# Performance work log

Hardware: AMD Instinct MI355X
Metric: run time of the kernel (lower is better)

The kernel has to match this reference:

```python
import jax, jax.numpy as jnp
import numpy as np

# Model/config constants (match init_kwargs)
B, S, D, H = 2, 2048, 512, 8
HD = D // H            # head dim = 64
WIN, DIL, G = 16, 2, 64  # window size, dilation rate, num global tokens
L = S - G              # 1984 local tokens (global indices are 0..G-1)


def setup_inputs() -> dict:
    key = jax.random.key(0)
    ks = jax.random.split(key, 16)
    sc = 0.02
    n = jax.random.normal
    return {
        "query": n(ks[0], (B, S, D), jnp.float32),
        "key": n(ks[1], (B, S, D), jnp.float32),
        "value": n(ks[2], (B, S, D), jnp.float32),
        # local multi-head attention params (linear_query/key/value/out_proj)
        "wq": n(ks[3], (D, D), jnp.float32) * sc, "bq": jnp.zeros((D,), jnp.float32),
        "wk": n(ks[4], (D, D), jnp.float32) * sc, "bk": jnp.zeros((D,), jnp.float32),
        "wv": n(ks[5], (D, D), jnp.float32) * sc, "bv": jnp.zeros((D,), jnp.float32),
        "wo": n(ks[6], (D, D), jnp.float32) * sc, "bo": jnp.zeros((D,), jnp.float32),
        # global nn.MultiheadAttention params (packed in_proj + out_proj)
        "g_in_w": n(ks[7], (3 * D, D), jnp.float32) * sc,
        "g_in_b": jnp.zeros((3 * D,), jnp.float32),
        "g_out_w": n(ks[8], (D, D), jnp.float32) * sc,
        "g_out_b": jnp.zeros((D,), jnp.float32),
    }


def _window_indices():
    # centered dilated window per local position, clipped to valid range
    pos = jnp.arange(L)
    offs = DIL * (jnp.arange(WIN) - WIN // 2)
    return jnp.clip(pos[:, None] + offs[None, :], 0, L - 1)


def reference(query, key, value, wq, bq, wk, bk, wv, bv, wo, bo,
              g_in_w, g_in_b, g_out_w, g_out_b):
    scale = 1.0 / np.sqrt(HD).astype(np.float32)

    # ---- local (dilated sliding window) path over tokens G..S-1 ----
    q_loc = query[:, G:, :]                      # (B, L, D)
    widx = _window_indices()
    k_win = key[:, G:, :][:, widx, :]
    v_win = value[:, G:, :][:, widx, :]

    q = (q_loc @ wq.T + bq).reshape(B, L, H, HD)          # (B,L,H,HD)
    k = (k_win @ wk.T + bk).reshape(B, L, WIN, H, HD)     # (B,L,W,H,HD)
    v = (v_win @ wv.T + bv).reshape(B, L, WIN, H, HD)

    scores = jnp.einsum('blhd,blwhd->blhw', q, k) * scale
    p = jax.nn.softmax(scores, axis=-1)
    o = jnp.einsum('blhw,blwhd->blhd', p, v).reshape(B, L, D)
    local_out = o @ wo.T + bo                              # (B,L,D)

    # ---- global token path: standard MHA over the G global tokens ----
    wq_g, wk_g, wv_g = g_in_w[:D], g_in_w[D:2 * D], g_in_w[2 * D:]
    bq_g, bk_g, bv_g = g_in_b[:D], g_in_b[D:2 * D], g_in_b[2 * D:]
    qg = (query[:, :G] @ wq_g.T + bq_g).reshape(B, G, H, HD)
    kg = (key[:, :G] @ wk_g.T + bk_g).reshape(B, G, H, HD)
    vg = (value[:, :G] @ wv_g.T + bv_g).reshape(B, G, H, HD)
    sg = jnp.einsum('bqhd,bkhd->bhqk', qg, kg) * scale     # (B,H,G,G)
    pg = jax.nn.softmax(sg, axis=-1)
    og = jnp.einsum('bhqk,bkhd->bqhd', pg, vg).reshape(B, G, D)
    global_out = og @ g_out_w.T + g_out_b                  # (B,G,D)

    # ---- fuse: scatter local + global back into full sequence ----
    out = jnp.zeros((B, S, D), query.dtype)
    out = out.at[:, G:, :].set(local_out)
    out = out.at[:, :G, :].set(global_out)
    return out
```

## Files before the change

### kernel.cpp

```cpp
#include <hip/hip_runtime.h>
#include <stdint.h>

#define B_ 2
#define S_ 2048
#define D_ 512
#define H_ 8
#define WIN_ 16
#define DIL_ 2
#define G_ 64
#define L_ (S_ - G_)

typedef short bf16x8 __attribute__((ext_vector_type(8)));
typedef float f32x4 __attribute__((ext_vector_type(4)));
typedef unsigned short u16;

#define LDSW 40

__device__ __forceinline__ float bf2f(u16 h) {
  return __uint_as_float(((uint32_t)h) << 16);
}
__device__ __forceinline__ u16 f2bf(float f) {
  uint32_t u = __float_as_uint(f);
  uint32_t r = (u + 0x7fffu + ((u >> 16) & 1u)) >> 16;
  return (u16)r;
}
__device__ __forceinline__ uint32_t pack2(float lo, float hi) {
  return (uint32_t)f2bf(lo) | ((uint32_t)f2bf(hi) << 16);
}

struct Job {
  const void* X; const float* W; const float* bias; void* Y;
  int rpb;
  int xoff;
  long xbs;
  int yoff;
  long ybs;
  int out_f32;
};
struct GemmLaunch { int start[6]; Job job[6]; };

template <int X_BF16>
__global__ __launch_bounds__(256) void gemm_kernel(GemmLaunch a) {
  int bid = (int)blockIdx.x;
  bid = (bid & 7) * ((int)gridDim.x >> 3) + (bid >> 3);

  int j = 0;
#pragma unroll
  for (int i = 1; i < 6; ++i) j = (bid >= a.start[i]) ? i : j;
  const Job jb = a.job[j];
  bid -= a.start[j];
  const int tm = bid >> 3, tn = bid & 7;
  const int row0 = tm * 128, n0 = tn * 64;

  __shared__ __align__(16) u16 As[2][128 * LDSW];
  __shared__ __align__(16) u16 Bs[2][64 * LDSW];

  const int tid = threadIdx.x, lane = tid & 63, w = tid >> 6;
  const int wm = w >> 1, wn = w & 1;

  const int rs = tid >> 2;
  const int kq = (tid & 3) * 8;

  const int r0 = row0 + rs,      b0 = r0 >= jb.rpb;
  const int r1 = row0 + 64 + rs, b1 = r1 >= jb.rpb;
  const size_t xi0 = (size_t)(b0 ? jb.xbs : 0) +
                     (size_t)(jb.xoff + r0 - (b0 ? jb.rpb : 0)) * 512 + kq;
  const size_t xi1 = (size_t)(b1 ? jb.xbs : 0) +
                     (size_t)(jb.xoff + r1 - (b1 ? jb.rpb : 0)) * 512 + kq;
  const float* wb0 = jb.W + (size_t)(n0 + rs) * 512 + kq;

  f32x4 acc[4][2];
#pragma unroll
  for (int i = 0; i < 4; ++i)
#pragma unroll
    for (int k = 0; k < 2; ++k) acc[i][k] = (f32x4){0.f, 0.f, 0.f, 0.f};

  f32x4 Aa0, Aa1, Aa2, Aa3, Aw0, Aw1;
  f32x4 Ba0, Ba1, Ba2, Ba3, Bw0, Bw1;
  int4  Ax0, Ax1, Bx0, Bx1;

  auto issueA = [&](int kof) {
    if constexpr (X_BF16) {
      const u16* xb = (const u16*)jb.X;
      Ax0 = *(const int4*)&xb[xi0 + kof];
      Ax1 = *(const int4*)&xb[xi1 + kof];
    } else {
      const float* xf = (const float*)jb.X;
      Aa0 = *(const f32x4*)(xf + xi0 + kof);
      Aa1 = *(const f32x4*)(xf + xi0 + kof + 4);
      Aa2 = *(const f32x4*)(xf + xi1 + kof);
      Aa3 = *(const f32x4*)(xf + xi1 + kof + 4);
    }
    Aw0 = *(const f32x4*)(wb0 + kof);
    Aw1 = *(const f32x4*)(wb0 + kof + 4);
  };
  auto issueB = [&](int kof) {
    if constexpr (X_BF16) {
      const u16* xb = (const u16*)jb.X;
      Bx0 = *(const int4*)&xb[xi0 + kof];
      Bx1 = *(const int4*)&xb[xi1 + kof];
    } else {
      const float* xf = (const float*)jb.X;
      Ba0 = *(const f32x4*)(xf + xi0 + kof);
      Ba1 = *(const f32x4*)(xf + xi0 + kof + 4);
      Ba2 = *(const f32x4*)(xf + xi1 + kof);
      Ba3 = *(const f32x4*)(xf + xi1 + kof + 4);
    }
    Bw0 = *(const f32x4*)(wb0 + kof);
    Bw1 = *(const f32x4*)(wb0 + kof + 4);
  };
  auto writeA = [&](int buf) {
    if constexpr (X_BF16) {
      *(int4*)&As[buf][rs * LDSW + kq]        = Ax0;
      *(int4*)&As[buf][(64 + rs) * LDSW + kq] = Ax1;
    } else {
      int4 p;
      p.x = (int)pack2(Aa0[0], Aa0[1]); p.y = (int)pack2(Aa0[2], Aa0[3]);
      p.z = (int)pack2(Aa1[0], Aa1[1]); p.w = (int)pack2(Aa1[2], Aa1[3]);
      *(int4*)&As[buf][rs * LDSW + kq] = p;
      p.x = (int)pack2(Aa2[0], Aa2[1]); p.y = (int)pack2(Aa2[2], Aa2[3]);
      p.z = (int)pack2(Aa3[0], Aa3[1]); p.w = (int)pack2(Aa3[2], Aa3[3]);
      *(int4*)&As[buf][(64 + rs) * LDSW + kq] = p;
    }
    int4 pw;
    pw.x = (int)pack2(Aw0[0], Aw0[1]); pw.y = (int)pack2(Aw0[2], Aw0[3]);
    pw.z = (int)pack2(Aw1[0], Aw1[1]); pw.w = (int)pack2(Aw1[2], Aw1[3]);
    *(int4*)&Bs[buf][rs * LDSW + kq] = pw;
  };
  auto writeB = [&](int buf) {
    if constexpr (X_BF16) {
      *(int4*)&As[buf][rs * LDSW + kq]        = Bx0;
      *(int4*)&As[buf][(64 + rs) * LDSW + kq] = Bx1;
    } else {
      int4 p;
      p.x = (int)pack2(Ba0[0], Ba0[1]); p.y = (int)pack2(Ba0[2], Ba0[3]);
      p.z = (int)pack2(Ba1[0], Ba1[1]); p.w = (int)pack2(Ba1[2], Ba1[3]);
      *(int4*)&As[buf][rs * LDSW + kq] = p;
      p.x = (int)pack2(Ba2[0], Ba2[1]); p.y = (int)pack2(Ba2[2], Ba2[3]);
      p.z = (int)pack2(Ba3[0], Ba3[1]); p.w = (int)pack2(Ba3[2], Ba3[3]);
      *(int4*)&As[buf][(64 + rs) * LDSW + kq] = p;
    }
    int4 pw;
    pw.x = (int)pack2(Bw0[0], Bw0[1]); pw.y = (int)pack2(Bw0[2], Bw0[3]);
    pw.z = (int)pack2(Bw1[0], Bw1[1]); pw.w = (int)pack2(Bw1[2], Bw1[3]);
    *(int4*)&Bs[buf][rs * LDSW + kq] = pw;
  };
  auto compute = [&](int buf) {
    bf16x8 af[4], bfv[2];
#pragma unroll
    for (int fm = 0; fm < 4; ++fm)
      af[fm] = *(const bf16x8*)&As[buf][(wm * 64 + fm * 16 + (lane & 15)) * LDSW + 8 * (lane >> 4)];
#pragma unroll
    for (int fn = 0; fn < 2; ++fn)
      bfv[fn] = *(const bf16x8*)&Bs[buf][(wn * 32 + fn * 16 + (lane & 15)) * LDSW + 8 * (lane >> 4)];
#pragma unroll
    for (int fm = 0; fm < 4; ++fm)
#pragma unroll
      for (int fn = 0; fn < 2; ++fn)
        acc[fm][fn] = __builtin_amdgcn_mfma_f32_16x16x32_bf16(af[fm], bfv[fn], acc[fm][fn], 0, 0, 0);
  };

  issueA(0);
  issueB(32);
  writeA(0);
  __syncthreads();
  for (int t = 0; t < 14; t += 2) {
    issueA((t + 2) * 32);
    compute(0);
    writeB(1);
    __syncthreads();
    issueB((t + 3) * 32);
    compute(1);
    writeA(0);
    __syncthreads();
  }
  compute(0);
  writeB(1);
  __syncthreads();
  compute(1);

#pragma unroll
  for (int fm = 0; fm < 4; ++fm) {
#pragma unroll
    for (int fn = 0; fn < 2; ++fn) {
#pragma unroll
      for (int r = 0; r < 4; ++r) {
        const int row = row0 + wm * 64 + fm * 16 + (lane >> 4) * 4 + r;
        const int col = n0 + wn * 32 + fn * 16 + (lane & 15);
        const int b = row >= jb.rpb;
        const int rr = row - (b ? jb.rpb : 0);
        const size_t yi = (size_t)(b ? jb.ybs : 0) + (size_t)(jb.yoff + rr) * 512 + col;
        const float v = acc[fm][fn][r] + jb.bias[col];
        if (jb.out_f32) ((float*)jb.Y)[yi] = v;
        else            ((u16*)jb.Y)[yi]   = f2bf(v);
      }
    }
  }
}

__global__ __launch_bounds__(256) void attn_kernel(const u16* qp, const u16* kp,
                                                   const u16* vp, u16* ob,
                                                   const u16* qgp, const u16* kgp,
                                                   const u16* vgp, u16* ogp) {
  const int lane = threadIdx.x & 63;
  int bid = (int)blockIdx.x;
  const int nbl = (B_ * L_) / 4;
  if (bid < nbl) bid = (bid & 7) * (nbl >> 3) + (bid >> 3);
  const int wid = bid * 4 + (threadIdx.x >> 6);

  if (wid < B_ * L_) {
    const int l = wid % L_;
    const int brow = wid - l;
    float q[8];
    {
      bf16x8 qv = *(const bf16x8*)&qp[(size_t)wid * 512 + lane * 8];
#pragma unroll
      for (int e = 0; e < 8; ++e) q[e] = bf2f((u16)qv[e]);
    }
    float s[WIN_];
#pragma unroll
    for (int w2 = 0; w2 < WIN_; ++w2) {
      int ki = l + DIL_ * w2 - WIN_;
      ki = ki < 0 ? 0 : (ki > L_ - 1 ? L_ - 1 : ki);
      bf16x8 kv = *(const bf16x8*)&kp[(size_t)(brow + ki) * 512 + lane * 8];
      float p = 0.f;
#pragma unroll
      for (int e = 0; e < 8; ++e) p = fmaf(q[e], bf2f((u16)kv[e]), p);
      p += __shfl_xor(p, 1); p += __shfl_xor(p, 2); p += __shfl_xor(p, 4);
      s[w2] = p * 0.125f;
    }
    float m = s[0];
#pragma unroll
    for (int w2 = 1; w2 < WIN_; ++w2) m = fmaxf(m, s[w2]);
    float sum = 0.f;
#pragma unroll
    for (int w2 = 0; w2 < WIN_; ++w2) { s[w2] = __expf(s[w2] - m); sum += s[w2]; }
    const float inv = 1.0f / sum;
    float acc[8] = {0.f};
#pragma unroll
    for (int w2 = 0; w2 < WIN_; ++w2) {
      int ki = l + DIL_ * w2 - WIN_;
      ki = ki < 0 ? 0 : (ki > L_ - 1 ? L_ - 1 : ki);
      bf16x8 vv = *(const bf16x8*)&vp[(size_t)(brow + ki) * 512 + lane * 8];
#pragma unroll
      for (int e = 0; e < 8; ++e) acc[e] = fmaf(s[w2], bf2f((u16)vv[e]), acc[e]);
    }
    bf16x8 o8;
#pragma unroll
    for (int e = 0; e < 8; ++e) o8[e] = (short)f2bf(acc[e] * inv);
    *(bf16x8*)&ob[(size_t)wid * 512 + lane * 8] = o8;
  } else {
    const int g = wid - B_ * L_;
    const int base = (g >> 6) * 64;
    const int qi = g & 63;
    float q[8];
    {
      bf16x8 qv = *(const bf16x8*)&qgp[(size_t)(base + qi) * 512 + lane * 8];
#pragma unroll
      for (int e = 0; e < 8; ++e) q[e] = bf2f((u16)qv[e]);
    }
    float m = -1e30f, sum = 0.f, acc[8] = {0.f};
    for (int j2 = 0; j2 < 64; ++j2) {
      bf16x8 kv = *(const bf16x8*)&kgp[(size_t)(base + j2) * 512 + lane * 8];
      float p = 0.f;
#pragma unroll
      for (int e = 0; e < 8; ++e) p = fmaf(q[e], bf2f((u16)kv[e]), p);
      p += __shfl_xor(p, 1); p += __shfl_xor(p, 2); p += __shfl_xor(p, 4);
      p *= 0.125f;
      const float mn = fmaxf(m, p);
      const float c  = __expf(m - mn);
      const float pe = __expf(p - mn);
      sum = sum * c + pe;
      m = mn;
      bf16x8 vv = *(const bf16x8*)&vgp[(size_t)(base + j2) * 512 + lane * 8];
#pragma unroll
      for (int e = 0; e < 8; ++e) acc[e] = acc[e] * c + pe * bf2f((u16)vv[e]);
    }
    const float inv = 1.0f / sum;
    bf16x8 o8;
#pragma unroll
    for (int e = 0; e < 8; ++e) o8[e] = (short)f2bf(acc[e] * inv);
    *(bf16x8*)&ogp[(size_t)(base + qi) * 512 + lane * 8] = o8;
  }
}

extern "C" void kernel_launch(void* const* d_in, const int* in_sizes, int n_in,
                              void* d_out, int out_size, void* d_ws, size_t ws_size,
                              hipStream_t stream) {
  const float* query   = (const float*)d_in[0];
  const float* key     = (const float*)d_in[1];
  const float* value   = (const float*)d_in[2];
  const float* wq      = (const float*)d_in[3];
  const float* bq      = (const float*)d_in[4];
  const float* wk      = (const float*)d_in[5];
  const float* bk      = (const float*)d_in[6];
  const float* wv      = (const float*)d_in[7];
  const float* bv      = (const float*)d_in[8];
  const float* wo      = (const float*)d_in[9];
  const float* bo      = (const float*)d_in[10];
  const float* g_in_w  = (const float*)d_in[11];
  const float* g_in_b  = (const float*)d_in[12];
  const float* g_out_w = (const float*)d_in[13];
  const float* g_out_b = (const float*)d_in[14];
  float* out = (float*)d_out;

  u16* w16 = (u16*)d_ws;
  const size_t PSZ = (size_t)B_ * L_ * D_;
  const size_t GSZ = (size_t)B_ * G_ * D_;

  u16* qp  = w16;        u16* kp  = qp + PSZ;   u16* vp  = kp + PSZ;
  u16* ob  = vp + PSZ;
  u16* qgp = ob + PSZ;   u16* kgp = qgp + GSZ;  u16* vgp = kgp + GSZ;
  u16* ogp = vgp + GSZ;

  const long XBS = (long)S_ * D_;
  const long PBS = (long)L_ * D_;
  const long GBS = (long)G_ * D_;

  GemmLaunch gi;
  gi.start[0] = 0; gi.start[1] = 248; gi.start[2] = 496;
  gi.start[3] = 744; gi.start[4] = 752; gi.start[5] = 760;
  gi.job[0] = {query, wq, bq, qp, L_, G_, XBS, 0, PBS, 0};
  gi.job[1] = {key,   wk, bk, kp, L_, G_, XBS, 0, PBS, 0};
  gi.job[2] = {value, wv, bv, vp, L_, G_, XBS, 0, PBS, 0};
  gi.job[3] = {query, g_in_w,             g_in_b,          qgp, G_, 0, XBS, 0, GBS, 0};
  gi.job[4] = {key,   g_in_w + 512 * D_,  g_in_b + D_,     kgp, G_, 0, XBS, 0, GBS, 0};
  gi.job[5] = {value, g_in_w + 1024 * D_, g_in_b + 2 * D_, vgp, G_, 0, XBS, 0, GBS, 0};
  hipLaunchKernelGGL(gemm_kernel<0>, dim3(768), dim3(256), 0, stream, gi);

  hipLaunchKernelGGL(attn_kernel, dim3((B_ * L_ + 128) / 4), dim3(256), 0, stream,
                     qp, kp, vp, ob, qgp, kgp, vgp, ogp);

  GemmLaunch go;
  go.start[0] = 0; go.start[1] = 248;
  go.start[2] = go.start[3] = go.start[4] = go.start[5] = 0x7fffffff;
  go.job[0] = {ob,  wo,      bo,      out, L_, 0, PBS, G_, XBS, 1};
  go.job[1] = {ogp, g_out_w, g_out_b, out, G_, 0, GBS, 0,  XBS, 1};
  go.job[2] = go.job[1]; go.job[3] = go.job[1]; go.job[4] = go.job[1]; go.job[5] = go.job[1];
  hipLaunchKernelGGL(gemm_kernel<1>, dim3(256), dim3(256), 0, stream, go);
}
```

Before: 162.2 us.

## Widen input-projection GEMM tile to 128x128 with 512-thread blocks

Adds a WIDE template variant of the GEMM where each 512-thread block computes a 128x128 output tile, with eight waves arranged 2x4, instead of 128x64 with 256 threads. Each thread now loads one A row and one W row per stage. The QKV input projections use it with half as many blocks, which raises reuse of A per block and halves redundant fp32 A loads and bf16 conversions. The compute section and epilogue are not shown, so it is unclear whether they handle the 4-wide wn mapping correctly. Fewer, larger blocks may also lower occupancy.

After: 162.9 us. About the same (+0.4%).

```diff
diff --git a/kernel.cpp b/kernel.cpp
--- a/kernel.cpp
+++ b/kernel.cpp
@@ -39,8 +39,8 @@
 };
 struct GemmLaunch { int start[6]; Job job[6]; };
 
-template <int X_BF16>
-__global__ __launch_bounds__(256) void gemm_kernel(GemmLaunch a) {
+template <int X_BF16, int WIDE>
+__global__ __launch_bounds__(WIDE ? 512 : 256) void gemm_kernel(GemmLaunch a) {
   int bid = (int)blockIdx.x;
   bid = (bid & 7) * ((int)gridDim.x >> 3) + (bid >> 3);
 
@@ -49,22 +49,24 @@
   for (int i = 1; i < 6; ++i) j = (bid >= a.start[i]) ? i : j;
   const Job jb = a.job[j];
   bid -= a.start[j];
-  const int tm = bid >> 3, tn = bid & 7;
-  const int row0 = tm * 128, n0 = tn * 64;
+  const int tm = WIDE ? (bid >> 2) : (bid >> 3);
+  const int tn = WIDE ? (bid & 3) : (bid & 7);
+  const int row0 = tm * 128, n0 = tn * (WIDE ? 128 : 64);
 
   __shared__ __align__(16) u16 As[2][128 * LDSW];
-  __shared__ __align__(16) u16 Bs[2][64 * LDSW];
+  __shared__ __align__(16) u16 Bs[2][(WIDE ? 128 : 64) * LDSW];
 
   const int tid = threadIdx.x, lane = tid & 63, w = tid >> 6;
-  const int wm = w >> 1, wn = w & 1;
+  const int wm = WIDE ? (w >> 2) : (w >> 1);
+  const int wn = WIDE ? (w & 3) : (w & 1);
 
   const int rs = tid >> 2;
   const int kq = (tid & 3) * 8;
 
   const int r0 = row0 + rs,      b0 = r0 >= jb.rpb;
-  const int r1 = row0 + 64 + rs, b1 = r1 >= jb.rpb;
   const size_t xi0 = (size_t)(b0 ? jb.xbs : 0) +
                      (size_t)(jb.xoff + r0 - (b0 ? jb.rpb : 0)) * 512 + kq;
+  const int r1 = row0 + 64 + rs, b1 = r1 >= jb.rpb;
   const size_t xi1 = (size_t)(b1 ? jb.xbs : 0) +
                      (size_t)(jb.xoff + r1 - (b1 ? jb.rpb : 0)) * 512 + kq;
   const float* wb0 = jb.W + (size_t)(n0 + rs) * 512 + kq;
@@ -83,13 +85,15 @@
     if constexpr (X_BF16) {
       const u16* xb = (const u16*)jb.X;
       Ax0 = *(const int4*)&xb[xi0 + kof];
-      Ax1 = *(const int4*)&xb[xi1 + kof];
+      if constexpr (!WIDE) Ax1 = *(const int4*)&xb[xi1 + kof];
     } else {
       const float* xf = (const float*)jb.X;
       Aa0 = *(const f32x4*)(xf + xi0 + kof);
       Aa1 = *(const f32x4*)(xf + xi0 + kof + 4);
-      Aa2 = *(const f32x4*)(xf + xi1 + kof);
-      Aa3 = *(const f32x4*)(xf + xi1 + kof + 4);
+      if constexpr (!WIDE) {
+        Aa2 = *(const f32x4*)(xf + xi1 + kof);
+        Aa3 = *(const f32x4*)(xf + xi1 + kof + 4);
+      }
     }
     Aw0 = *(const f32x4*)(wb0 + kof);
     Aw1 = *(const f32x4*)(wb0 + kof + 4);
@@ -98,29 +102,33 @@
     if constexpr (X_BF16) {
       const u16* xb = (const u16*)jb.X;
       Bx0 = *(const int4*)&xb[xi0 + kof];
-      Bx1 = *(const int4*)&xb[xi1 + kof];
+      if constexpr (!WIDE) Bx1 = *(const int4*)&xb[xi1 + kof];
     } else {
       const float* xf = (const float*)jb.X;
       Ba0 = *(const f32x4*)(xf + xi0 + kof);
       Ba1 = *(const f32x4*)(xf + xi0 + kof + 4);
-      Ba2 = *(const f32x4*)(xf + xi1 + kof);
-      Ba3 = *(const f32x4*)(xf + xi1 + kof + 4);
+      if constexpr (!WIDE) {
+        Ba2 = *(const f32x4*)(xf + xi1 + kof);
+        Ba3 = *(const f32x4*)(xf + xi1 + kof + 4);
+      }
     }
     Bw0 = *(const f32x4*)(wb0 + kof);
     Bw1 = *(const f32x4*)(wb0 + kof + 4);
   };
   auto writeA = [&](int buf) {
     if constexpr (X_BF16) {
-      *(int4*)&As[buf][rs * LDSW + kq]        = Ax0;
-      *(int4*)&As[buf][(64 + rs) * LDSW + kq] = Ax1;
+      *(int4*)&As[buf][rs * LDSW + kq] = Ax0;
+      if constexpr (!WIDE) *(int4*)&As[buf][(64 + rs) * LDSW + kq] = Ax1;
     } else {
       int4 p;
       p.x = (int)pack2(Aa0[0], Aa0[1]); p.y = (int)pack2(Aa0[2], Aa0[3]);
       p.z = (int)pack2(Aa1[0], Aa1[1]); p.w = (int)pack2(Aa1[2], Aa1[3]);
       *(int4*)&As[buf][rs * LDSW + kq] = p;
-      p.x = (int)pack2(Aa2[0], Aa2[1]); p.y = (int)pack2(Aa2[2], Aa2[3]);
-      p.z = (int)pack2(Aa3[0], Aa3[1]); p.w = (int)pack2(Aa3[2], Aa3[3]);
-      *(int4*)&As[buf][(64 + rs) * LDSW + kq] = p;
+      if constexpr (!WIDE) {
+        p.x = (int)pack2(Aa2[0], Aa2[1]); p.y = (int)pack2(Aa2[2], Aa2[3]);
+        p.z = (int)pack2(Aa3[0], Aa3[1]); p.w = (int)pack2(Aa3[2], Aa3[3]);
+        *(int4*)&As[buf][(64 + rs) * LDSW + kq] = p;
+      }
     }
     int4 pw;
     pw.x = (int)pack2(Aw0[0], Aw0[1]); pw.y = (int)pack2(Aw0[2], Aw0[3]);
@@ -129,16 +137,18 @@
   };
   auto writeB = [&](int buf) {
     if constexpr (X_BF16) {
-      *(int4*)&As[buf][rs * LDSW + kq]        = Bx0;
-      *(int4*)&As[buf][(64 + rs) * LDSW + kq] = Bx1;
+      *(int4*)&As[buf][rs * LDSW + kq] = Bx0;
+      if constexpr (!WIDE) *(int4*)&As[buf][(64 + rs) * LDSW + kq] = Bx1;
     } else {
       int4 p;
       p.x = (int)pack2(Ba0[0], Ba0[1]); p.y = (int)pack2(Ba0[2], Ba0[3]);
       p.z = (int)pack2(Ba1[0], Ba1[1]); p.w = (int)pack2(Ba1[2], Ba1[3]);
       *(int4*)&As[buf][rs * LDSW + kq] = p;
-      p.x = (int)pack2(Ba2[0], Ba2[1]); p.y = (int)pack2(Ba2[2], Ba2[3]);
-      p.z = (int)pack2(Ba3[0], Ba3[1]); p.w = (int)pack2(Ba3[2], Ba3[3]);
-      *(int4*)&As[buf][(64 + rs) * LDSW + kq] = p;
+      if constexpr (!WIDE) {
+        p.x = (int)pack2(Ba2[0], Ba2[1]); p.y = (int)pack2(Ba2[2], Ba2[3]);
+        p.z = (int)pack2(Ba3[0], Ba3[1]); p.w = (int)pack2(Ba3[2], Ba3[3]);
+        *(int4*)&As[buf][(64 + rs) * LDSW + kq] = p;
+      }
     }
     int4 pw;
     pw.x = (int)pack2(Bw0[0], Bw0[1]); pw.y = (int)pack2(Bw0[2], Bw0[3]);
@@ -318,15 +328,15 @@
   const long GBS = (long)G_ * D_;
 
   GemmLaunch gi;
-  gi.start[0] = 0; gi.start[1] = 248; gi.start[2] = 496;
-  gi.start[3] = 744; gi.start[4] = 752; gi.start[5] = 760;
+  gi.start[0] = 0; gi.start[1] = 124; gi.start[2] = 248;
+  gi.start[3] = 372; gi.start[4] = 376; gi.start[5] = 380;
   gi.job[0] = {query, wq, bq, qp, L_, G_, XBS, 0, PBS, 0};
   gi.job[1] = {key,   wk, bk, kp, L_, G_, XBS, 0, PBS, 0};
   gi.job[2] = {value, wv, bv, vp, L_, G_, XBS, 0, PBS, 0};
   gi.job[3] = {query, g_in_w,             g_in_b,          qgp, G_, 0, XBS, 0, GBS, 0};
   gi.job[4] = {key,   g_in_w + 512 * D_,  g_in_b + D_,     kgp, G_, 0, XBS, 0, GBS, 0};
   gi.job[5] = {value, g_in_w + 1024 * D_, g_in_b + 2 * D_, vgp, G_, 0, XBS, 0, GBS, 0};
-  hipLaunchKernelGGL(gemm_kernel<0>, dim3(768), dim3(256), 0, stream, gi);
+  hipLaunchKernelGGL((gemm_kernel<0, 1>), dim3(384), dim3(512), 0, stream, gi);
 
   hipLaunchKernelGGL(attn_kernel, dim3((B_ * L_ + 128) / 4), dim3(256), 0, stream,
                      qp, kp, vp, ob, qgp, kgp, vgp, ogp);
@@ -337,5 +347,5 @@
   go.job[0] = {ob,  wo,      bo,      out, L_, 0, PBS, G_, XBS, 1};
   go.job[1] = {ogp, g_out_w, g_out_b, out, G_, 0, GBS, 0,  XBS, 1};
   go.job[2] = go.job[1]; go.job[3] = go.job[1]; go.job[4] = go.job[1]; go.job[5] = go.job[1];
-  hipLaunchKernelGGL(gemm_kernel<1>, dim3(256), dim3(256), 0, stream, go);
-}
+  hipLaunchKernelGGL((gemm_kernel<1, 0>), dim3(256), dim3(256), 0, stream, go);
+}
```
